# Performance work log

Measured on AMD Instinct MI355X. Metric: run time of the kernel, lower is better.

Reference implementation:

```python
import jax, jax.numpy as jnp
import numpy as np

BIG_K, SMALL_K = 13, 3
NK = -(-BIG_K // SMALL_K)  # 5
NUM_PATHS = 3
BN_EPS = 1e-5


def _shifts():
    mid = BIG_K // 2
    pad = SMALL_K - 1
    return [-(mid - i * SMALL_K - pad) for i in range(NK)]  # [-4,-1,2,5,8]


def _conv1x1(x, w):
    return jax.lax.conv_general_dilated(
        x, w, window_strides=(1, 1), padding='VALID',
        dimension_numbers=('NCHW', 'OIHW', 'NCHW'))


def _dwconv3x3(x, w, groups):
    # x: (b, groups, h, w); w: (groups, 1, 3, 3)
    return jax.lax.conv_general_dilated(
        x, w, window_strides=(1, 1), padding=[(1, 1), (1, 1)],
        dimension_numbers=('NCHW', 'OIHW', 'NCHW'),
        feature_group_count=groups)


def setup_inputs() -> dict:
    key = jax.random.key(0)
    ks = jax.random.split(key, 8)
    b, c1, c2, h, w = 16, 256, 256, 64, 64
    return {
        'x': jax.random.normal(ks[0], (b, c1, h, w), jnp.float32),
        'w_expand': jax.random.normal(ks[1], (c2 * NK, c1, 1, 1), jnp.float32) * 0.05,
        'w_path': jax.random.normal(ks[2], (NUM_PATHS, NK, c2, 1, 3, 3), jnp.float32) * 0.1,
        'w_mix': jax.random.normal(ks[3], (c2, c2, 1, 1), jnp.float32) * 0.05,
        'bn_gamma': jnp.ones((c2,), jnp.float32),
        'bn_beta': jnp.zeros((c2,), jnp.float32),
        'bn_mean': jnp.zeros((c2,), jnp.float32),
        'bn_var': jnp.ones((c2,), jnp.float32),
    }


def reference(x, w_expand, w_path, w_mix, bn_gamma, bn_beta, bn_mean, bn_var):
    b, c1, h, w = x.shape
    c2 = w_mix.shape[0]
    # 1) channel expand: c1 -> c2*nk (1x1 conv, big GEMM)
    x_exp = _conv1x1(x, w_expand)                      # (b, c2*NK, h, w)
    x_r = x_exp.reshape(b, c2, NK, h, w)
    # 2) roll each shift group; conv is linear in kernel, so summing over the
    #    3 paths of depthwise weights gives identical math to summing outputs.
    shifts = _shifts()
    rolled = jnp.stack(
        [jnp.roll(x_r[:, :, k], (shifts[k], shifts[k]), axis=(2, 3)) for k in range(NK)],
        axis=2)                                        # (b, c2, NK, h, w)
    rolled_flat = rolled.reshape(b, c2 * NK, h, w)      # channel layout: c2-major, nk-minor
    w_eff = jnp.sum(w_path, axis=0)                     # (NK, c2, 1, 3, 3)
    w_flat = jnp.transpose(w_eff, (1, 0, 2, 3, 4)).reshape(c2 * NK, 1, 3, 3)
    conv_out = _dwconv3x3(rolled_flat, w_flat, groups=c2 * NK)
    merged = conv_out.reshape(b, c2, NK, h, w).sum(axis=2)  # sum over shifts (paths already folded)
    # 3) channel mix + BN (inference) + SiLU
    out = _conv1x1(merged, w_mix)
    inv = jax.lax.rsqrt(bn_var + BN_EPS)
    out = (out - bn_mean[None, :, None, None]) * (bn_gamma * inv)[None, :, None, None] + bn_beta[None, :, None, None]
    return out * jax.nn.sigmoid(out)  # SiLU
```

## Files before the change

### kernel.cpp

```cpp
#include <hip/hip_runtime.h>
#include <hip/hip_bf16.h>
#include <math.h>

#define NB   16
#define C1   256
#define C2   256
#define NK   5
#define NEXP (C2 * NK)
#define HW   4096

typedef __attribute__((ext_vector_type(8))) short bf16x8;
typedef __attribute__((ext_vector_type(4))) float f32x4;

__device__ __forceinline__ unsigned short bfbits(float v) {
    return __builtin_bit_cast(unsigned short, __float2bfloat16(v));
}

#define LGKM_BARRIER() do { \
    asm volatile("s_waitcnt lgkmcnt(0)" ::: "memory"); \
    __builtin_amdgcn_sched_barrier(0); \
    __builtin_amdgcn_s_barrier(); } while (0)

__global__ void weff_kernel(const float* __restrict__ w_path, float* __restrict__ weff) {
    int idx = blockIdx.x * 256 + threadIdx.x;
    if (idx >= NK * C2 * 9) return;
    float s = 0.f;
    #pragma unroll
    for (int p = 0; p < 3; ++p)
        s += w_path[(long)p * NK * C2 * 9 + idx];
    weff[idx] = s;
}

__global__ void cvt_bf16_kernel(const float* __restrict__ in, __hip_bfloat16* __restrict__ out, int n) {
    int i = blockIdx.x * 256 + threadIdx.x;
    if (i < n) out[i] = __float2bfloat16(in[i]);
}

template <int NCH, bool FP32B, bool OUT_BF16>
__global__ __launch_bounds__(512, 2)
void nstream_gemm_kernel(const __hip_bfloat16* __restrict__ A,
                         const void* __restrict__ B_all,
                         void* __restrict__ C_all,
                         long bStrideB, long bStrideC, int bOffB, int bOffC,
                         const float* __restrict__ bn_gamma, const float* __restrict__ bn_beta,
                         const float* __restrict__ bn_mean, const float* __restrict__ bn_var) {
    constexpr int KK = 256, NN = 4096;
    __shared__ __align__(16) char Bs[2][64 * 512];
    const int z  = blockIdx.z;
    const int nBase = blockIdx.x * (64 * NCH);
    const int m0 = blockIdx.y * 256;
    const int t  = threadIdx.x;
    const int lane = t & 63;
    const int wv = t >> 6;
    const int lr = lane & 15, lg = lane >> 4;

    bf16x8 af[2][8];
    const __hip_bfloat16* wp = A + (long)(m0 + wv * 32 + lr) * KK + lg * 8;
    #pragma unroll
    for (int s = 0; s < 2; ++s)
        #pragma unroll
        for (int ks = 0; ks < 8; ++ks)
            af[s][ks] = *(const bf16x8*)(wp + (long)s * 16 * KK + ks * 32);

    float scl[2], mnv[2], btv[2];
    if constexpr (!OUT_BF16) {
        #pragma unroll
        for (int s = 0; s < 2; ++s) {
            const int m = m0 + wv * 32 + s * 16 + lr;
            scl[s] = bn_gamma[m] * rsqrtf(bn_var[m] + 1e-5f);
            mnv[s] = bn_mean[m];
            btv[s] = bn_beta[m];
        }
    }

    const int sn = t & 63;
    const int kb = (t >> 6) * 32;
    const int key = sn & 31;
    const char* Bbase = (const char*)B_all + (long)(bOffB + z) * bStrideB * (FP32B ? 4 : 2);

    float    fr[32];
    unsigned hr[32];

    auto issueB = [&](int ci) {
        const int nc = nBase + ci * 64 + sn;
        #pragma unroll
        for (int gq = 0; gq < 2; ++gq) {
            if constexpr (FP32B) {
                const float* p = (const float*)Bbase + (long)(kb + gq * 16) * NN + nc;
                #pragma unroll
                for (int i = 0; i < 16; ++i) fr[gq * 16 + i] = p[(long)i * NN];
            } else {
                const unsigned short* p = (const unsigned short*)Bbase + (long)(kb + gq * 16) * NN + nc;
                #pragma unroll
                for (int i = 0; i < 16; ++i) hr[gq * 16 + i] = p[(long)i * NN];
            }
        }
    };
    auto writeB = [&](int ci) {
        char* buf = Bs[ci & 1];
        #pragma unroll
        for (int gq = 0; gq < 2; ++gq) {
            unsigned u[8];
            #pragma unroll
            for (int i = 0; i < 8; ++i) {
                if constexpr (FP32B)
                    u[i] = (unsigned)bfbits(fr[gq * 16 + 2 * i]) |
                           ((unsigned)bfbits(fr[gq * 16 + 2 * i + 1]) << 16);
                else
                    u[i] = (hr[gq * 16 + 2 * i] & 0xffffu) | (hr[gq * 16 + 2 * i + 1] << 16);
            }
            const int ch0 = (kb >> 3) + gq * 2;
            *(uint4*)(buf + sn * 512 + ((ch0 ^ key) * 16))       = *(uint4*)&u[0];
            *(uint4*)(buf + sn * 512 + (((ch0 + 1) ^ key) * 16)) = *(uint4*)&u[4];
        }
    };

    issueB(0);
    writeB(0);
    LGKM_BARRIER();

    #pragma unroll
    for (int ci = 0; ci < NCH; ++ci) {
        if (ci + 1 < NCH) {
            issueB(ci + 1);
            __builtin_amdgcn_sched_barrier(0);
        }
        char* buf = Bs[ci & 1];

        f32x4 acc[2][4];
        #pragma unroll
        for (int s = 0; s < 2; ++s)
            #pragma unroll
            for (int j = 0; j < 4; ++j)
                acc[s][j] = (f32x4){0.f, 0.f, 0.f, 0.f};

        __builtin_amdgcn_s_setprio(1);
        #pragma unroll
        for (int ks = 0; ks < 8; ++ks) {
            #pragma unroll
            for (int j = 0; j < 4; ++j) {
                const int n = j * 16 + lr;
                bf16x8 bfr = *(const bf16x8*)(buf + n * 512 + (((ks * 4 + lg) ^ (n & 31)) * 16));
                acc[0][j] = __builtin_amdgcn_mfma_f32_16x16x32_bf16(bfr, af[0][ks], acc[0][j], 0, 0, 0);
                acc[1][j] = __builtin_amdgcn_mfma_f32_16x16x32_bf16(bfr, af[1][ks], acc[1][j], 0, 0, 0);
            }
        }
        __builtin_amdgcn_s_setprio(0);

        const int ncb = nBase + ci * 64;
        if constexpr (OUT_BF16) {
            if (ci + 1 < NCH) writeB(ci + 1);
            __hip_bfloat16* C = (__hip_bfloat16*)C_all + (long)(bOffC + z) * bStrideC;
            #pragma unroll
            for (int s = 0; s < 2; ++s) {
                const int m = m0 + wv * 32 + s * 16 + lr;
                #pragma unroll
                for (int j = 0; j < 4; ++j) {
                    const long n = ncb + j * 16 + lg * 4;
                    short4 sv;
                    sv.x = (short)bfbits(acc[s][j][0]);
                    sv.y = (short)bfbits(acc[s][j][1]);
                    sv.z = (short)bfbits(acc[s][j][2]);
                    sv.w = (short)bfbits(acc[s][j][3]);
                    *(short4*)(C + (long)m * NN + n) = sv;
                }
            }
            if (ci + 1 < NCH) LGKM_BARRIER();
        } else {
            float* C = (float*)C_all + (long)(bOffC + z) * bStrideC;
            LGKM_BARRIER();
            #pragma unroll
            for (int h = 0; h < 2; ++h) {
                if ((wv >> 2) == h) {
                    #pragma unroll
                    for (int s = 0; s < 2; ++s) {
                        const int mrel = (wv & 3) * 32 + s * 16 + lr;
                        const int kx = (mrel & 7) << 4;
                        #pragma unroll
                        for (int j = 0; j < 4; ++j) {
                            const int nb = j * 64 + lg * 16;
                            float4 v;
                            float t0 = (acc[s][j][0] - mnv[s]) * scl[s] + btv[s];
                            float t1 = (acc[s][j][1] - mnv[s]) * scl[s] + btv[s];
                            float t2 = (acc[s][j][2] - mnv[s]) * scl[s] + btv[s];
                            float t3 = (acc[s][j][3] - mnv[s]) * scl[s] + btv[s];
                            v.x = t0 / (1.0f + __expf(-t0));
                            v.y = t1 / (1.0f + __expf(-t1));
                            v.z = t2 / (1.0f + __expf(-t2));
                            v.w = t3 / (1.0f + __expf(-t3));
                            *(float4*)(buf + mrel * 256 + (nb ^ kx)) = v;
                        }
                    }
                }
                LGKM_BARRIER();
                #pragma unroll
                for (int i = 0; i < 4; ++i) {
                    const int p = i * 8192 + t * 16;
                    const int mrel = p >> 8;
                    const int w = p & 255;
                    uint4 v = *(uint4*)(buf + mrel * 256 + (w ^ ((mrel & 7) << 4)));
                    *(uint4*)((char*)(C + (long)(m0 + h * 128 + mrel) * NN + ncb) + w) = v;
                }
                LGKM_BARRIER();
            }
            if (ci + 1 < NCH) {
                writeB(ci + 1);
                LGKM_BARRIER();
            }
        }
    }
}

__global__ __launch_bounds__(256)
void shift_dw_kernel(const __hip_bfloat16* __restrict__ xexp,
                     const float* __restrict__ weff,
                     __hip_bfloat16* __restrict__ merged) {
    __shared__ __align__(16) __hip_bfloat16 sd[NK * 34 * 64];
    const int t  = threadIdx.x;
    const int r0 = blockIdx.x * 32;
    const int c  = blockIdx.y;
    const int z  = blockIdx.z;
    const int shifts[NK] = {-4, -1, 2, 5, 8};
    const __hip_bfloat16* base = xexp + ((long)z * NEXP + (long)c * NK) * HW;

    for (int idx = t; idx < NK * 34 * 8; idx += 256) {
        int k   = idx / (34 * 8);
        int rem = idx - k * (34 * 8);
        int rr  = rem >> 3, ch = (rem & 7) * 8;
        int grow = (r0 - 1 + rr - shifts[k]) & 63;
        *(bf16x8*)&sd[(k * 34 + rr) * 64 + ch] =
            *(const bf16x8*)(base + (long)k * HW + grow * 64 + ch);
    }
    __syncthreads();

    const int j  = t & 63;
    const int ty = t >> 6;
    const int pbase = ty * 8;
    const bool topEdge = (r0 == 0)  && (ty == 0);
    const bool botEdge = (r0 == 32) && (ty == 3);

    float2 acc[4];
    #pragma unroll
    for (int i = 0; i < 4; ++i) acc[i] = (float2){0.f, 0.f};

    #pragma unroll
    for (int k = 0; k < NK; ++k) {
        const int s = shifts[k];
        const int cL = (j - 1 - s) & 63;
        const int cC = (j - s) & 63;
        const int cR = (j + 1 - s) & 63;
        const float* wp = &weff[((long)k * C2 + c) * 9];
        float w[9];
        #pragma unroll
        for (int i = 0; i < 9; ++i) w[i] = wp[i];
        if (j == 0)  { w[0] = 0.f; w[3] = 0.f; w[6] = 0.f; }
        if (j == 63) { w[2] = 0.f; w[5] = 0.f; w[8] = 0.f; }
        const __hip_bfloat16* pl = &sd[k * 34 * 64];

        float vL[4], vC[4], vR[4];
        #pragma unroll
        for (int w4 = 0; w4 < 4; ++w4) {
            vL[w4] = __bfloat162float(pl[(pbase + w4) * 64 + cL]);
            vC[w4] = __bfloat162float(pl[(pbase + w4) * 64 + cC]);
            vR[w4] = __bfloat162float(pl[(pbase + w4) * 64 + cR]);
        }
        if (topEdge) { vL[0] = 0.f; vC[0] = 0.f; vR[0] = 0.f; }

        #pragma unroll
        for (int pr = 0; pr < 4; ++pr) {
            #pragma unroll
            for (int u = 0; u < 3; ++u) {
                const int wi  = (2 * pr + u) & 3;
                const int wi2 = (2 * pr + u + 1) & 3;
                acc[pr].x += w[u*3+0] * vL[wi]  + w[u*3+1] * vC[wi]  + w[u*3+2] * vR[wi];
                acc[pr].y += w[u*3+0] * vL[wi2] + w[u*3+1] * vC[wi2] + w[u*3+2] * vR[wi2];
            }
            if (pr < 3) {
                const int na = (2 * pr) & 3, nb = (2 * pr + 1) & 3;
                const int ra = pbase + 2 * pr + 4, rb = pbase + 2 * pr + 5;
                vL[na] = __bfloat162float(pl[ra * 64 + cL]);
                vC[na] = __bfloat162float(pl[ra * 64 + cC]);
                vR[na] = __bfloat162float(pl[ra * 64 + cR]);
                vL[nb] = __bfloat162float(pl[rb * 64 + cL]);
                vC[nb] = __bfloat162float(pl[rb * 64 + cC]);
                vR[nb] = __bfloat162float(pl[rb * 64 + cR]);
                if (botEdge && pr == 2) { vL[nb] = 0.f; vC[nb] = 0.f; vR[nb] = 0.f; }
            }
        }
    }

    long outb = ((long)z * C2 + c) * HW + (long)(r0 + ty * 8) * 64 + j;
    #pragma unroll
    for (int pr = 0; pr < 4; ++pr) {
        merged[outb + (long)(2 * pr) * 64]     = __float2bfloat16(acc[pr].x);
        merged[outb + (long)(2 * pr + 1) * 64] = __float2bfloat16(acc[pr].y);
    }
}

extern "C" void kernel_launch(void* const* d_in, const int* in_sizes, int n_in,
                              void* d_out, int out_size, void* d_ws, size_t ws_size,
                              hipStream_t stream) {
    const float* x        = (const float*)d_in[0];
    const float* w_expand = (const float*)d_in[1];
    const float* w_path   = (const float*)d_in[2];
    const float* w_mix    = (const float*)d_in[3];
    const float* bn_gamma = (const float*)d_in[4];
    const float* bn_beta  = (const float*)d_in[5];
    const float* bn_mean  = (const float*)d_in[6];
    const float* bn_var   = (const float*)d_in[7];

    char* ws = (char*)d_ws;
    float* weff             = (float*)ws;
    __hip_bfloat16* wexp_bf = (__hip_bfloat16*)(ws + 65536);
    __hip_bfloat16* wmix_bf = (__hip_bfloat16*)(ws + 65536 + 655360);
    const size_t head = 1 << 20;

    const size_t xe_per = (size_t)NEXP * HW * 2;
    const size_t mg_per = (size_t)C2 * HW * 2;
    const size_t per_b = xe_per + mg_per;

    int g = 1;
    if (ws_size > head + per_b) {
        size_t fit = (ws_size - head) / per_b;
        g = (int)(fit < NB ? fit : NB);
        if (g < 1) g = 1;
    }

    char* p = ws + head;
    __hip_bfloat16* xexp   = (__hip_bfloat16*)p; p += (size_t)g * xe_per;
    __hip_bfloat16* merged = (__hip_bfloat16*)p;

    weff_kernel<<<(NK * C2 * 9 + 255) / 256, 256, 0, stream>>>(w_path, weff);
    cvt_bf16_kernel<<<(NEXP * C1 + 255) / 256, 256, 0, stream>>>(w_expand, wexp_bf, NEXP * C1);
    cvt_bf16_kernel<<<(C2 * C2 + 255) / 256, 256, 0, stream>>>(w_mix, wmix_bf, C2 * C2);

    for (int b0 = 0; b0 < NB; b0 += g) {
        int gb = (NB - b0) < g ? (NB - b0) : g;
        nstream_gemm_kernel<4, true, true><<<dim3(HW / 256, NEXP / 256, gb), 512, 0, stream>>>(
            wexp_bf, x, xexp,
            (long)C1 * HW, (long)NEXP * HW, b0, 0,
            nullptr, nullptr, nullptr, nullptr);
        shift_dw_kernel<<<dim3(2, C2, gb), 256, 0, stream>>>(xexp, weff, merged);
        nstream_gemm_kernel<2, false, false><<<dim3(HW / 128, 1, gb), 512, 0, stream>>>(
            wmix_bf, merged, d_out,
            (long)C2 * HW, (long)C2 * HW, 0, b0,
            bn_gamma, bn_beta, bn_mean, bn_var);
    }
}
```

Baseline: 239.2 us.

## Remap expand GEMM blocks per XCD for B reuse; async LDS loads in shift kernel

After: 243.0 us. Within noise of the previous version (+1.6%).

```diff
diff --git a/kernel.cpp b/kernel.cpp
--- a/kernel.cpp
+++ b/kernel.cpp
@@ -12,6 +12,10 @@
 typedef __attribute__((ext_vector_type(8))) short bf16x8;
 typedef __attribute__((ext_vector_type(4))) float f32x4;
 
+#define GLOAD_LDS16(g, l) __builtin_amdgcn_global_load_lds( \
+    (const __attribute__((address_space(1))) void*)(g), \
+    (__attribute__((address_space(3))) void*)(l), 16, 0, 0)
+
 __device__ __forceinline__ unsigned short bfbits(float v) {
     return __builtin_bit_cast(unsigned short, __float2bfloat16(v));
 }
@@ -36,19 +40,29 @@
     if (i < n) out[i] = __float2bfloat16(in[i]);
 }
 
-template <int NCH, bool FP32B, bool OUT_BF16>
+template <int NCH, bool FP32B, bool OUT_BF16, bool GROUPED>
 __global__ __launch_bounds__(512, 2)
 void nstream_gemm_kernel(const __hip_bfloat16* __restrict__ A,
                          const void* __restrict__ B_all,
-                         void* __restrict__ C_all,
+                         void* __restrict__ C_all, int zCount,
                          long bStrideB, long bStrideC, int bOffB, int bOffC,
                          const float* __restrict__ bn_gamma, const float* __restrict__ bn_beta,
                          const float* __restrict__ bn_mean, const float* __restrict__ bn_var) {
     constexpr int KK = 256, NN = 4096;
     __shared__ __align__(16) char Bs[2][64 * 512];
-    const int z  = blockIdx.z;
-    const int nBase = blockIdx.x * (64 * NCH);
-    const int m0 = blockIdx.y * 256;
+    int nBase, m0, zz;
+    if constexpr (GROUPED) {
+        const int w = blockIdx.x, xcd = w & 7, j = w >> 3;
+        const int Gl = j / 5, member = j - 5 * Gl;
+        const int G = xcd * 4 * zCount + Gl;
+        nBase = (G & 31) * (64 * NCH);
+        zz = G >> 5;
+        m0 = member * 256;
+    } else {
+        nBase = blockIdx.x * (64 * NCH);
+        m0 = blockIdx.y * 256;
+        zz = blockIdx.z;
+    }
     const int t  = threadIdx.x;
     const int lane = t & 63;
     const int wv = t >> 6;
@@ -76,7 +90,7 @@
     const int sn = t & 63;
     const int kb = (t >> 6) * 32;
     const int key = sn & 31;
-    const char* Bbase = (const char*)B_all + (long)(bOffB + z) * bStrideB * (FP32B ? 4 : 2);
+    const char* Bbase = (const char*)B_all + (long)(bOffB + zz) * bStrideB * (FP32B ? 4 : 2);
 
     float    fr[32];
     unsigned hr[32];
@@ -150,7 +164,7 @@
         const int ncb = nBase + ci * 64;
         if constexpr (OUT_BF16) {
             if (ci + 1 < NCH) writeB(ci + 1);
-            __hip_bfloat16* C = (__hip_bfloat16*)C_all + (long)(bOffC + z) * bStrideC;
+            __hip_bfloat16* C = (__hip_bfloat16*)C_all + (long)(bOffC + zz) * bStrideC;
             #pragma unroll
             for (int s = 0; s < 2; ++s) {
                 const int m = m0 + wv * 32 + s * 16 + lr;
@@ -167,7 +181,7 @@
             }
             if (ci + 1 < NCH) LGKM_BARRIER();
         } else {
-            float* C = (float*)C_all + (long)(bOffC + z) * bStrideC;
+            float* C = (float*)C_all + (long)(bOffC + zz) * bStrideC;
             LGKM_BARRIER();
             #pragma unroll
             for (int h = 0; h < 2; ++h) {
@@ -223,13 +237,16 @@
     const int shifts[NK] = {-4, -1, 2, 5, 8};
     const __hip_bfloat16* base = xexp + ((long)z * NEXP + (long)c * NK) * HW;
 
-    for (int idx = t; idx < NK * 34 * 8; idx += 256) {
-        int k   = idx / (34 * 8);
-        int rem = idx - k * (34 * 8);
-        int rr  = rem >> 3, ch = (rem & 7) * 8;
-        int grow = (r0 - 1 + rr - shifts[k]) & 63;
-        *(bf16x8*)&sd[(k * 34 + rr) * 64 + ch] =
-            *(const bf16x8*)(base + (long)k * HW + grow * 64 + ch);
+    #pragma unroll
+    for (int i = 0; i < 6; ++i) {
+        const int idx = t + i * 256;
+        if (idx < NK * 34 * 8) {
+            const int k   = idx / 272;
+            const int rem = idx - k * 272;
+            const int rr  = rem >> 3, ch = (rem & 7) * 8;
+            const int grow = (r0 - 1 + rr - shifts[k]) & 63;
+            GLOAD_LDS16(base + (long)k * HW + grow * 64 + ch, (char*)sd + idx * 16);
+        }
     }
     __syncthreads();
 
@@ -336,13 +353,13 @@
 
     for (int b0 = 0; b0 < NB; b0 += g) {
         int gb = (NB - b0) < g ? (NB - b0) : g;
-        nstream_gemm_kernel<4, true, true><<<dim3(HW / 256, NEXP / 256, gb), 512, 0, stream>>>(
-            wexp_bf, x, xexp,
+        nstream_gemm_kernel<2, true, true, true><<<dim3(160 * gb), 512, 0, stream>>>(
+            wexp_bf, x, xexp, gb,
             (long)C1 * HW, (long)NEXP * HW, b0, 0,
             nullptr, nullptr, nullptr, nullptr);
         shift_dw_kernel<<<dim3(2, C2, gb), 256, 0, stream>>>(xexp, weff, merged);
-        nstream_gemm_kernel<2, false, false><<<dim3(HW / 128, 1, gb), 512, 0, stream>>>(
-            wmix_bf, merged, d_out,
+        nstream_gemm_kernel<2, false, false, false><<<dim3(HW / 128, 1, gb), 512, 0, stream>>>(
+            wmix_bf, merged, d_out, gb,
             (long)C2 * HW, (long)C2 * HW, 0, b0,
             bn_gamma, bn_beta, bn_mean, bn_var);
     }
```

## Fold roll shifts into expand GEMM epilogue and stage depthwise tile as fp32

Applied to the files above, without the earlier changes.

Result: slower. 287.7 us (+20.3%).

```diff
diff --git a/kernel.cpp b/kernel.cpp
--- a/kernel.cpp
+++ b/kernel.cpp
@@ -154,15 +154,19 @@
             #pragma unroll
             for (int s = 0; s < 2; ++s) {
                 const int m = m0 + wv * 32 + s * 16 + lr;
+                const int sh = 3 * (m % 5) - 4;
+                __hip_bfloat16* Cm = C + (long)m * NN;
                 #pragma unroll
-                for (int j = 0; j < 4; ++j) {
-                    const long n = ncb + j * 16 + lg * 4;
-                    short4 sv;
-                    sv.x = (short)bfbits(acc[s][j][0]);
-                    sv.y = (short)bfbits(acc[s][j][1]);
-                    sv.z = (short)bfbits(acc[s][j][2]);
-                    sv.w = (short)bfbits(acc[s][j][3]);
-                    *(short4*)(C + (long)m * NN + n) = sv;
+                for (int jf = 0; jf < 4; ++jf) {
+                    const int n = ncb + jf * 16 + lg * 4;
+                    const int row = n >> 6, col = n & 63;
+                    __hip_bfloat16* Cr = Cm + ((row + sh) & 63) * 64;
+                    #pragma unroll
+                    for (int e = 0; e < 4; ++e) {
+                        __hip_bfloat16 hv;
+                        hv = __float2bfloat16(acc[s][jf][e]);
+                        Cr[(col + sh + e) & 63] = hv;
+                    }
                 }
             }
             if (ci + 1 < NCH) LGKM_BARRIER();
@@ -215,21 +219,38 @@
 void shift_dw_kernel(const __hip_bfloat16* __restrict__ xexp,
                      const float* __restrict__ weff,
                      __hip_bfloat16* __restrict__ merged) {
-    __shared__ __align__(16) __hip_bfloat16 sd[NK * 34 * 64];
+    __shared__ __align__(16) float sdbuf[4 + NK * 34 * 64 + 4];
+    float* const sd = sdbuf + 4;
     const int t  = threadIdx.x;
     const int r0 = blockIdx.x * 32;
     const int c  = blockIdx.y;
     const int z  = blockIdx.z;
-    const int shifts[NK] = {-4, -1, 2, 5, 8};
     const __hip_bfloat16* base = xexp + ((long)z * NEXP + (long)c * NK) * HW;
 
-    for (int idx = t; idx < NK * 34 * 8; idx += 256) {
-        int k   = idx / (34 * 8);
-        int rem = idx - k * (34 * 8);
-        int rr  = rem >> 3, ch = (rem & 7) * 8;
-        int grow = (r0 - 1 + rr - shifts[k]) & 63;
-        *(bf16x8*)&sd[(k * 34 + rr) * 64 + ch] =
-            *(const bf16x8*)(base + (long)k * HW + grow * 64 + ch);
+    bf16x8 rawv[6];
+    int loc[6];
+    #pragma unroll
+    for (int i = 0; i < 6; ++i) {
+        const int idx = t + i * 256;
+        if (idx < NK * 34 * 8) {
+            const int k   = idx / 272;
+            const int rem = idx - k * 272;
+            const int rr  = rem >> 3, ch = (rem & 7) * 8;
+            const int grow = (r0 - 1 + rr) & 63;
+            rawv[i] = *(const bf16x8*)(base + (long)k * HW + grow * 64 + ch);
+            loc[i] = (k * 34 + rr) * 64 + ch;
+        } else loc[i] = -1;
+    }
+    #pragma unroll
+    for (int i = 0; i < 6; ++i) {
+        if (loc[i] >= 0) {
+            float f[8];
+            #pragma unroll
+            for (int e = 0; e < 8; ++e)
+                f[e] = __uint_as_float(((unsigned)(unsigned short)rawv[i][e]) << 16);
+            *(float4*)&sd[loc[i]]     = (float4){f[0], f[1], f[2], f[3]};
+            *(float4*)&sd[loc[i] + 4] = (float4){f[4], f[5], f[6], f[7]};
+        }
     }
     __syncthreads();
 
@@ -245,24 +266,19 @@
 
     #pragma unroll
     for (int k = 0; k < NK; ++k) {
-        const int s = shifts[k];
-        const int cL = (j - 1 - s) & 63;
-        const int cC = (j - s) & 63;
-        const int cR = (j + 1 - s) & 63;
         const float* wp = &weff[((long)k * C2 + c) * 9];
         float w[9];
         #pragma unroll
         for (int i = 0; i < 9; ++i) w[i] = wp[i];
         if (j == 0)  { w[0] = 0.f; w[3] = 0.f; w[6] = 0.f; }
         if (j == 63) { w[2] = 0.f; w[5] = 0.f; w[8] = 0.f; }
-        const __hip_bfloat16* pl = &sd[k * 34 * 64];
+        const float* pl = sd + k * (34 * 64) + j;
 
         float vL[4], vC[4], vR[4];
         #pragma unroll
         for (int w4 = 0; w4 < 4; ++w4) {
-            vL[w4] = __bfloat162float(pl[(pbase + w4) * 64 + cL]);
-            vC[w4] = __bfloat162float(pl[(pbase + w4) * 64 + cC]);
-            vR[w4] = __bfloat162float(pl[(pbase + w4) * 64 + cR]);
+            const float* rp = pl + (pbase + w4) * 64;
+            vL[w4] = rp[-1]; vC[w4] = rp[0]; vR[w4] = rp[1];
         }
         if (topEdge) { vL[0] = 0.f; vC[0] = 0.f; vR[0] = 0.f; }
 
@@ -277,13 +293,10 @@
             }
             if (pr < 3) {
                 const int na = (2 * pr) & 3, nb = (2 * pr + 1) & 3;
-                const int ra = pbase + 2 * pr + 4, rb = pbase + 2 * pr + 5;
-                vL[na] = __bfloat162float(pl[ra * 64 + cL]);
-                vC[na] = __bfloat162float(pl[ra * 64 + cC]);
-                vR[na] = __bfloat162float(pl[ra * 64 + cR]);
-                vL[nb] = __bfloat162float(pl[rb * 64 + cL]);
-                vC[nb] = __bfloat162float(pl[rb * 64 + cC]);
-                vR[nb] = __bfloat162float(pl[rb * 64 + cR]);
+                const float* ra = pl + (pbase + 2 * pr + 4) * 64;
+                const float* rb = pl + (pbase + 2 * pr + 5) * 64;
+                vL[na] = ra[-1]; vC[na] = ra[0]; vR[na] = ra[1];
+                vL[nb] = rb[-1]; vC[nb] = rb[0]; vR[nb] = rb[1];
                 if (botEdge && pr == 2) { vL[nb] = 0.f; vC[nb] = 0.f; vR[nb] = 0.f; }
             }
         }
```

## Restructure shift depthwise kernel: full-plane tiles, direct-to-LDS loads, 2x4 register blocking

Applied to the files above, without the earlier changes.

Result: faster. 201.3 us (median of 2 runs) (-15.8%).

```diff
diff --git a/kernel.cpp b/kernel.cpp
--- a/kernel.cpp
+++ b/kernel.cpp
@@ -12,9 +12,15 @@
 typedef __attribute__((ext_vector_type(8))) short bf16x8;
 typedef __attribute__((ext_vector_type(4))) float f32x4;
 
+#define GLOAD_LDS16(g, l) __builtin_amdgcn_global_load_lds( \
+    (const __attribute__((address_space(1))) void*)(g), \
+    (__attribute__((address_space(3))) void*)(l), 16, 0, 0)
+
 __device__ __forceinline__ unsigned short bfbits(float v) {
     return __builtin_bit_cast(unsigned short, __float2bfloat16(v));
 }
+__device__ __forceinline__ float bflo(unsigned u) { return __uint_as_float(u << 16); }
+__device__ __forceinline__ float bfhi(unsigned u) { return __uint_as_float(u & 0xffff0000u); }
 
 #define LGKM_BARRIER() do { \
     asm volatile("s_waitcnt lgkmcnt(0)" ::: "memory"); \
@@ -211,89 +217,94 @@
     }
 }
 
-__global__ __launch_bounds__(256)
+__global__ __launch_bounds__(512)
 void shift_dw_kernel(const __hip_bfloat16* __restrict__ xexp,
                      const float* __restrict__ weff,
                      __hip_bfloat16* __restrict__ merged) {
-    __shared__ __align__(16) __hip_bfloat16 sd[NK * 34 * 64];
-    const int t  = threadIdx.x;
-    const int r0 = blockIdx.x * 32;
-    const int c  = blockIdx.y;
-    const int z  = blockIdx.z;
+    __shared__ __align__(16) __hip_bfloat16 sd[NK * 66 * 64];
+    const int t = threadIdx.x;
+    const int c = blockIdx.x;
+    const int z = blockIdx.y;
     const int shifts[NK] = {-4, -1, 2, 5, 8};
     const __hip_bfloat16* base = xexp + ((long)z * NEXP + (long)c * NK) * HW;
 
-    for (int idx = t; idx < NK * 34 * 8; idx += 256) {
-        int k   = idx / (34 * 8);
-        int rem = idx - k * (34 * 8);
-        int rr  = rem >> 3, ch = (rem & 7) * 8;
-        int grow = (r0 - 1 + rr - shifts[k]) & 63;
-        *(bf16x8*)&sd[(k * 34 + rr) * 64 + ch] =
-            *(const bf16x8*)(base + (long)k * HW + grow * 64 + ch);
+    if (t < 80) {
+        const int k = t >> 4, which = (t >> 3) & 1, ch = (t & 7) * 8;
+        bf16x8 zz = {};
+        *(bf16x8*)&sd[(k * 66 + which * 65) * 64 + ch] = zz;
+    }
+    #pragma unroll
+    for (int k = 0; k < NK; ++k) {
+        const int r  = t >> 3;
+        const int ch = (t & 7) * 8;
+        const int grow = (r - shifts[k]) & 63;
+        GLOAD_LDS16(base + (long)k * HW + grow * 64 + ch,
+                    (char*)sd + (k * 66 + 1) * 128 + t * 16);
     }
     __syncthreads();
 
-    const int j  = t & 63;
-    const int ty = t >> 6;
-    const int pbase = ty * 8;
-    const bool topEdge = (r0 == 0)  && (ty == 0);
-    const bool botEdge = (r0 == 32) && (ty == 3);
-
-    float2 acc[4];
-    #pragma unroll
-    for (int i = 0; i < 4; ++i) acc[i] = (float2){0.f, 0.f};
+    const int pairi = t & 31;
+    const int j2 = pairi * 2;
+    const int ty = t >> 5;
+    const int pbase = ty * 4;
+
+    f32x4 acc[2];
+    acc[0] = (f32x4){0.f, 0.f, 0.f, 0.f};
+    acc[1] = (f32x4){0.f, 0.f, 0.f, 0.f};
 
     #pragma unroll
     for (int k = 0; k < NK; ++k) {
         const int s = shifts[k];
-        const int cL = (j - 1 - s) & 63;
-        const int cC = (j - s) & 63;
-        const int cR = (j + 1 - s) & 63;
-        const float* wp = &weff[((long)k * C2 + c) * 9];
-        float w[9];
-        #pragma unroll
-        for (int i = 0; i < 9; ++i) w[i] = wp[i];
-        if (j == 0)  { w[0] = 0.f; w[3] = 0.f; w[6] = 0.f; }
-        if (j == 63) { w[2] = 0.f; w[5] = 0.f; w[8] = 0.f; }
-        const __hip_bfloat16* pl = &sd[k * 34 * 64];
-
-        float vL[4], vC[4], vR[4];
-        #pragma unroll
-        for (int w4 = 0; w4 < 4; ++w4) {
-            vL[w4] = __bfloat162float(pl[(pbase + w4) * 64 + cL]);
-            vC[w4] = __bfloat162float(pl[(pbase + w4) * 64 + cC]);
-            vR[w4] = __bfloat162float(pl[(pbase + w4) * 64 + cR]);
-        }
-        if (topEdge) { vL[0] = 0.f; vC[0] = 0.f; vR[0] = 0.f; }
-
-        #pragma unroll
-        for (int pr = 0; pr < 4; ++pr) {
+        const float* wpk = &weff[((long)k * C2 + c) * 9];
+        float wA[9], wB[9];
+        #pragma unroll
+        for (int i = 0; i < 9; ++i) { wA[i] = wpk[i]; wB[i] = wA[i]; }
+        if (j2 == 0)      { wA[0] = 0.f; wA[3] = 0.f; wA[6] = 0.f; }
+        if (j2 + 1 == 63) { wB[2] = 0.f; wB[5] = 0.f; wB[8] = 0.f; }
+        const int cin = (j2 - 1 - s) & 63;
+        const __hip_bfloat16* sdk = sd + k * (66 * 64);
+
+        float V0[4], V1[4], V2[4], V3[4];
+        auto LDR = [&](int rs, int slot) {
+            const __hip_bfloat16* rp = sdk + (pbase + rs) * 64;
+            if ((cin & 1) == 0) {
+                unsigned a = *(const unsigned*)(rp + cin);
+                unsigned b = *(const unsigned*)(rp + ((cin + 2) & 63));
+                V0[slot] = bflo(a); V1[slot] = bfhi(a);
+                V2[slot] = bflo(b); V3[slot] = bfhi(b);
+            } else {
+                unsigned a = *(const unsigned*)(rp + (cin & 62));
+                unsigned b = *(const unsigned*)(rp + ((cin + 1) & 63));
+                unsigned d = *(const unsigned*)(rp + ((cin + 3) & 63));
+                V0[slot] = bfhi(a);
+                V1[slot] = bflo(b); V2[slot] = bfhi(b);
+                V3[slot] = bflo(d);
+            }
+        };
+
+        LDR(0, 0); LDR(1, 1); LDR(2, 2); LDR(3, 3);
+        #pragma unroll
+        for (int pr = 0; pr < 2; ++pr) {
             #pragma unroll
             for (int u = 0; u < 3; ++u) {
-                const int wi  = (2 * pr + u) & 3;
-                const int wi2 = (2 * pr + u + 1) & 3;
-                acc[pr].x += w[u*3+0] * vL[wi]  + w[u*3+1] * vC[wi]  + w[u*3+2] * vR[wi];
-                acc[pr].y += w[u*3+0] * vL[wi2] + w[u*3+1] * vC[wi2] + w[u*3+2] * vR[wi2];
-            }
-            if (pr < 3) {
-                const int na = (2 * pr) & 3, nb = (2 * pr + 1) & 3;
-                const int ra = pbase + 2 * pr + 4, rb = pbase + 2 * pr + 5;
-                vL[na] = __bfloat162float(pl[ra * 64 + cL]);
-                vC[na] = __bfloat162float(pl[ra * 64 + cC]);
-                vR[na] = __bfloat162float(pl[ra * 64 + cR]);
-                vL[nb] = __bfloat162float(pl[rb * 64 + cL]);
-                vC[nb] = __bfloat162float(pl[rb * 64 + cC]);
-                vR[nb] = __bfloat162float(pl[rb * 64 + cR]);
-                if (botEdge && pr == 2) { vL[nb] = 0.f; vC[nb] = 0.f; vR[nb] = 0.f; }
-            }
-        }
-    }
-
-    long outb = ((long)z * C2 + c) * HW + (long)(r0 + ty * 8) * 64 + j;
-    #pragma unroll
-    for (int pr = 0; pr < 4; ++pr) {
-        merged[outb + (long)(2 * pr) * 64]     = __float2bfloat16(acc[pr].x);
-        merged[outb + (long)(2 * pr + 1) * 64] = __float2bfloat16(acc[pr].y);
+                const int iA = (2 * pr + u) & 3;
+                const int iB = (2 * pr + u + 1) & 3;
+                acc[pr][0] += wA[u*3] * V0[iA] + wA[u*3+1] * V1[iA] + wA[u*3+2] * V2[iA];
+                acc[pr][1] += wB[u*3] * V1[iA] + wB[u*3+1] * V2[iA] + wB[u*3+2] * V3[iA];
+                acc[pr][2] += wA[u*3] * V0[iB] + wA[u*3+1] * V1[iB] + wA[u*3+2] * V2[iB];
+                acc[pr][3] += wB[u*3] * V1[iB] + wB[u*3+1] * V2[iB] + wB[u*3+2] * V3[iB];
+            }
+            if (pr == 0) { LDR(4, 0); LDR(5, 1); }
+        }
+    }
+
+    __hip_bfloat16* out = merged + ((long)z * C2 + c) * HW + (long)pbase * 64 + j2;
+    #pragma unroll
+    for (int pr = 0; pr < 2; ++pr) {
+        unsigned ua = (unsigned)bfbits(acc[pr][0]) | ((unsigned)bfbits(acc[pr][1]) << 16);
+        unsigned ub = (unsigned)bfbits(acc[pr][2]) | ((unsigned)bfbits(acc[pr][3]) << 16);
+        *(unsigned*)(out + (long)(2 * pr) * 64)     = ua;
+        *(unsigned*)(out + (long)(2 * pr + 1) * 64) = ub;
     }
 }
 
@@ -340,7 +351,7 @@
             wexp_bf, x, xexp,
             (long)C1 * HW, (long)NEXP * HW, b0, 0,
             nullptr, nullptr, nullptr, nullptr);
-        shift_dw_kernel<<<dim3(2, C2, gb), 256, 0, stream>>>(xexp, weff, merged);
+        shift_dw_kernel<<<dim3(C2, gb), 512, 0, stream>>>(xexp, weff, merged);
         nstream_gemm_kernel<2, false, false><<<dim3(HW / 128, 1, gb), 512, 0, stream>>>(
             wmix_bf, merged, d_out,
             (long)C2 * HW, (long)C2 * HW, 0, b0,
```
